# Kernel tuning notes

Measured on AMD Instinct MI355X. Metric: run time of the kernel, lower is better.

The kernel has to match this reference:

```python
import jax, jax.numpy as jnp
import numpy as np

EPS = 1e-5

def group_norm(x, gamma, beta):
    # GroupNorm(1, C) on [N, C]: normalize over channel dim per sample
    mu = jnp.mean(x, axis=-1, keepdims=True)
    var = jnp.var(x, axis=-1, keepdims=True)
    return (x - mu) * jax.lax.rsqrt(var + EPS) * gamma + beta

def setup_inputs() -> dict:
    key = jax.random.key(0)
    ks = jax.random.split(key, 4)
    T, B, I, H = 2048, 64, 256, 512
    s1 = 1.0 / np.sqrt(H + I)
    s2 = 1.0 / np.sqrt(H)
    return {
        "input": jax.random.normal(ks[0], (T, B, I), dtype=jnp.float32),
        "W1": jax.random.uniform(ks[1], (H, H + I), jnp.float32, -s1, s1),
        "g1": jnp.ones((H,), jnp.float32), "b1": jnp.zeros((H,), jnp.float32),
        "W2": jax.random.uniform(ks[2], (H, H), jnp.float32, -s2, s2),
        "g2": jnp.ones((H,), jnp.float32), "b2": jnp.zeros((H,), jnp.float32),
        "W3": jax.random.uniform(ks[3], (3 * H, H), jnp.float32, -s2, s2),
        "g3": jnp.ones((3 * H,), jnp.float32), "b3": jnp.zeros((3 * H,), jnp.float32),
    }

def reference(input, W1, g1, b1, W2, g2, b2, W3, g3, b3):
    T, B, I = input.shape
    H = W1.shape[0]

    def step(c, x):
        z = jnp.concatenate([x, c], axis=1)              # [B, I+H]
        h = jax.nn.elu(group_norm(z @ W1.T, g1, b1))     # [B, H]
        h = jax.nn.elu(group_norm(h @ W2.T, g2, b2))     # [B, H]
        o = group_norm(h @ W3.T, g3, b3)                 # [B, 3H]
        new_hx, new_cx, forget = o[:, :H], o[:, H:2*H], o[:, 2*H:]
        f = jax.nn.sigmoid(forget) ** 2                  # sigmoid_pow(x, 2)
        retain = 1.0 - f
        hx = jax.nn.elu(new_hx)
        cx = jax.nn.elu(new_cx)
        c_new = f * cx + retain * c
        return c_new, hx

    c0 = jnp.zeros((B, H), dtype=input.dtype)
    c_final, outputs = jax.lax.scan(step, c0, input)
    return outputs, c_final[None]
```

## Files before the change

### kernel.cpp

```cpp
#include <hip/hip_runtime.h>
#include <math.h>

#define T_STEPS 2048
#define BATCH   64
#define IDIM    256
#define HDIM    512
#define K1      768
#define H3      1536
#define NGROUP  4
#define NSLICE  32
#define RPG     16
#define THREADS 512

#define OFF_A1  0
#define OFF_A2  32768
#define OFF_CB  65536
#define OFF_P3  98304
#define OFF_ST  102400

typedef __attribute__((ext_vector_type(8))) __bf16 bf16x8;
typedef __attribute__((ext_vector_type(4))) float f32x4;

__device__ __forceinline__ f32x4 MFMA(bf16x8 a, bf16x8 b, f32x4 c) {
    return __builtin_amdgcn_mfma_f32_16x16x32_bf16(a, b, c, 0, 0, 0);
}

__device__ __forceinline__ float gload(const float* p) {
    return __hip_atomic_load(p, __ATOMIC_RELAXED, __HIP_MEMORY_SCOPE_AGENT);
}
__device__ __forceinline__ void gstore(float* p, float v) {
    __hip_atomic_store(p, v, __ATOMIC_RELAXED, __HIP_MEMORY_SCOPE_AGENT);
}
__device__ __forceinline__ float2 gload2(const float* p) {
    unsigned long long v = __hip_atomic_load((const unsigned long long*)p,
                                             __ATOMIC_RELAXED, __HIP_MEMORY_SCOPE_AGENT);
    return __builtin_bit_cast(float2, v);
}
__device__ __forceinline__ void gstore2(float* p, float a, float b) {
    float2 v = {a, b};
    __hip_atomic_store((unsigned long long*)p, __builtin_bit_cast(unsigned long long, v),
                       __ATOMIC_RELAXED, __HIP_MEMORY_SCOPE_AGENT);
}
__device__ __forceinline__ int gload_i(const int* p) {
    return __hip_atomic_load(p, __ATOMIC_RELAXED, __HIP_MEMORY_SCOPE_AGENT);
}
__device__ __forceinline__ unsigned gload_u(const unsigned* p) {
    return __hip_atomic_load(p, __ATOMIC_RELAXED, __HIP_MEMORY_SCOPE_AGENT);
}
__device__ __forceinline__ void gstore_us(unsigned short* p, unsigned short v) {
    __hip_atomic_store(p, v, __ATOMIC_RELAXED, __HIP_MEMORY_SCOPE_AGENT);
}

struct bf16pair { __bf16 hi, lo; };
__device__ __forceinline__ bf16pair split2(float f) {
    bf16pair r;
    r.hi = (__bf16)f;
    r.lo = (__bf16)(f - (float)r.hi);
    return r;
}
__device__ __forceinline__ unsigned pk2(float a, float b) {
    return (unsigned)__builtin_bit_cast(unsigned short, (__bf16)a) |
           ((unsigned)__builtin_bit_cast(unsigned short, (__bf16)b) << 16);
}
__device__ __forceinline__ void st_pair(__bf16* p, __bf16 a, __bf16 b) {
    unsigned v = (unsigned)__builtin_bit_cast(unsigned short, a) |
                 ((unsigned)__builtin_bit_cast(unsigned short, b) << 16);
    *(unsigned*)p = v;
}
__device__ __forceinline__ float elu1(float v) {
    return v > 0.f ? v : (expf(v) - 1.f);
}

__device__ __forceinline__ void publish(int* stamp_s, int val) {
    __syncthreads();
    if (threadIdx.x == 0)
        __hip_atomic_store(stamp_s, val, __ATOMIC_RELAXED, __HIP_MEMORY_SCOPE_AGENT);
}
__device__ __forceinline__ void poll_wave(const int* st, int target) {
    const int* p = st + (threadIdx.x & 31);
    while (true) {
        int v = gload_i(p);
        if (__all(v >= target)) break;
        __builtin_amdgcn_s_sleep(1);
    }
}

__global__ void dlstm_init(float* __restrict__ ws) {
    int idx = threadIdx.x;
    if (idx < 512) ((int*)(ws + OFF_ST))[idx] = 0;
}

__global__ __launch_bounds__(THREADS, 2) void dlstm_main(
    const float* __restrict__ x,
    const float* __restrict__ W1, const float* __restrict__ g1, const float* __restrict__ b1,
    const float* __restrict__ W2, const float* __restrict__ g2, const float* __restrict__ b2,
    const float* __restrict__ W3, const float* __restrict__ g3, const float* __restrict__ b3,
    float* __restrict__ out, float* __restrict__ ws)
{
    const int tid = threadIdx.x;
    const int bid = blockIdx.x;
    const int g = bid & 3;
    const int s = bid >> 2;
    const int r0 = g * RPG;

    const int lane = tid & 63;
    const int wv   = tid >> 6;
    const int col  = lane & 15;
    const int kq   = lane >> 4;
    const int er   = tid >> 5;
    const int l32  = tid & 31;

    float* a1 = ws + OFF_A1;
    float* a2 = ws + OFF_A2;
    unsigned short* cbu = (unsigned short*)(ws + OFF_CB);
    float* p3 = ws + OFF_P3;
    int* stb   = (int*)(ws + OFF_ST);
    int* st_a1 = stb + 0   + g * 32;
    int* st_a2 = stb + 128 + g * 32;
    int* st_p3 = stb + 256 + g * 32;
    int* st_cb = stb + 384 + g * 32;

    __shared__ __bf16 zh[16][776];
    __shared__ float comb[8][3][256];
    __shared__ float slab[16][48];
    __shared__ float stats[16][2];

    float2 g1v[8], b1v[8], g2v[8], b2v[8];
    #pragma unroll
    for (int j = 0; j < 8; ++j) {
        int k = j * 64 + l32 * 2;
        g1v[j] = *(const float2*)(g1 + k); b1v[j] = *(const float2*)(b1 + k);
        g2v[j] = *(const float2*)(g2 + k); b2v[j] = *(const float2*)(b2 + k);
    }
    float g3h = 0.f, g3c = 0.f, g3f = 0.f, b3h = 0.f, b3c = 0.f, b3f = 0.f;
    if (tid < 256) {
        int i = tid & 15; int h = 16 * s + i;
        g3h = g3[h];        g3c = g3[HDIM + h];        g3f = g3[2 * HDIM + h];
        b3h = b3[h];        b3c = b3[HDIM + h];        b3f = b3[2 * HDIM + h];
    }

    bf16x8 w1h[3], w1l[3], w2h[2], w2l[2], w3h[3][2], w3l[3][2];
    #pragma unroll
    for (int ks = 0; ks < 3; ++ks) {
        int k0 = wv * 96 + ks * 32 + kq * 8;
        const float* p = W1 + (size_t)(16 * s + col) * K1 + k0;
        #pragma unroll
        for (int e = 0; e < 8; ++e) {
            bf16pair pr = split2(p[e]);
            w1h[ks][e] = pr.hi; w1l[ks][e] = pr.lo;
        }
    }
    #pragma unroll
    for (int ks = 0; ks < 2; ++ks) {
        int k0 = wv * 64 + ks * 32 + kq * 8;
        const float* p = W2 + (size_t)(16 * s + col) * HDIM + k0;
        #pragma unroll
        for (int e = 0; e < 8; ++e) {
            bf16pair pr = split2(p[e]);
            w2h[ks][e] = pr.hi; w2l[ks][e] = pr.lo;
        }
    }
    #pragma unroll
    for (int tb = 0; tb < 3; ++tb) {
        #pragma unroll
        for (int ks = 0; ks < 2; ++ks) {
            int k0 = wv * 64 + ks * 32 + kq * 8;
            const float* p = W3 + (size_t)(tb * HDIM + 16 * s + col) * HDIM + k0;
            #pragma unroll
            for (int e = 0; e < 8; ++e) {
                bf16pair pr = split2(p[e]);
                w3h[tb][ks][e] = pr.hi; w3l[tb][ks][e] = pr.lo;
            }
        }
    }

    float creg = 0.f;

    float2 xr[4];
    unsigned xb[4];
    {
        const float* xrow = x + (size_t)(r0 + er) * IDIM;
        #pragma unroll
        for (int j = 0; j < 4; ++j) xr[j] = *(const float2*)(xrow + j * 64 + l32 * 2);
        #pragma unroll
        for (int j = 0; j < 4; ++j) xb[j] = pk2(xr[j].x, xr[j].y);
    }

    #pragma unroll 1
    for (int t = 0; t < T_STEPS; ++t) {
        unsigned* zrow = (unsigned*)&zh[er][0];
        #pragma unroll
        for (int j = 0; j < 4; ++j) zrow[j * 32 + l32] = xb[j];
        __syncthreads();
        f32x4 acc = {0.f, 0.f, 0.f, 0.f};
        #pragma unroll
        for (int ks = 0; ks < 3; ++ks) {
            int kb = wv * 96 + ks * 32;
            if (kb < IDIM) {
                bf16x8 ah = *(const bf16x8*)&zh[col][kb + kq * 8];
                acc = MFMA(ah, w1h[ks], acc);
                acc = MFMA(ah, w1l[ks], acc);
            }
        }
        if (t > 0) {
            poll_wave(st_cb, t);
            const unsigned* cbrow = (const unsigned*)cbu + (size_t)(r0 + er) * (HDIM / 2);
            #pragma unroll
            for (int j = 0; j < 8; ++j)
                zrow[128 + j * 32 + l32] = gload_u(cbrow + j * 32 + l32);
        } else {
            #pragma unroll
            for (int j = 0; j < 8; ++j) zrow[128 + j * 32 + l32] = 0u;
        }
        __syncthreads();
        #pragma unroll
        for (int ks = 0; ks < 3; ++ks) {
            int kb = wv * 96 + ks * 32;
            if (kb >= IDIM) {
                bf16x8 ah = *(const bf16x8*)&zh[col][kb + kq * 8];
                acc = MFMA(ah, w1h[ks], acc);
                acc = MFMA(ah, w1l[ks], acc);
            }
        }
        #pragma unroll
        for (int i = 0; i < 4; ++i) comb[wv][0][(kq * 4 + i) * 16 + col] = acc[i];
        __syncthreads();
        if (tid < 128) {
            int r = tid >> 3, fp = tid & 7;
            int i0 = r * 16 + fp * 2;
            float v0 = 0.f, v1 = 0.f;
            #pragma unroll
            for (int w = 0; w < 8; ++w) { v0 += comb[w][0][i0]; v1 += comb[w][0][i0 + 1]; }
            gstore2(&a1[(size_t)(r0 + r) * HDIM + 16 * s + fp * 2], v0, v1);
        }
        publish(&st_a1[s], t + 1);

        poll_wave(st_a1, t + 1);
        {
            size_t arow = (size_t)(r0 + er) * HDIM;
            float2 va[8]; float s1 = 0.f, s2 = 0.f;
            #pragma unroll
            for (int j = 0; j < 8; ++j) {
                va[j] = gload2(a1 + arow + j * 64 + l32 * 2);
                s1 += va[j].x + va[j].y; s2 += va[j].x * va[j].x + va[j].y * va[j].y;
            }
            s1 += __shfl_xor(s1, 1, 64); s2 += __shfl_xor(s2, 1, 64);
            s1 += __shfl_xor(s1, 2, 64); s2 += __shfl_xor(s2, 2, 64);
            s1 += __shfl_xor(s1, 4, 64); s2 += __shfl_xor(s2, 4, 64);
            s1 += __shfl_xor(s1, 8, 64); s2 += __shfl_xor(s2, 8, 64);
            s1 += __shfl_xor(s1, 16, 64); s2 += __shfl_xor(s2, 16, 64);
            float mu = s1 * (1.f / HDIM);
            float var = s2 * (1.f / HDIM) - mu * mu;
            float rs = rsqrtf(var + 1e-5f);
            #pragma unroll
            for (int j = 0; j < 8; ++j) {
                int k = j * 64 + l32 * 2;
                float v0 = elu1((va[j].x - mu) * rs * g1v[j].x + b1v[j].x);
                float v1 = elu1((va[j].y - mu) * rs * g1v[j].y + b1v[j].y);
                st_pair(&zh[er][k], (__bf16)v0, (__bf16)v1);
            }
        }
        __syncthreads();
        {
            f32x4 acc2 = {0.f, 0.f, 0.f, 0.f};
            #pragma unroll
            for (int ks = 0; ks < 2; ++ks) {
                int k0 = wv * 64 + ks * 32 + kq * 8;
                bf16x8 ah = *(const bf16x8*)&zh[col][k0];
                acc2 = MFMA(ah, w2h[ks], acc2);
                acc2 = MFMA(ah, w2l[ks], acc2);
            }
            #pragma unroll
            for (int i = 0; i < 4; ++i) comb[wv][0][(kq * 4 + i) * 16 + col] = acc2[i];
        }
        __syncthreads();
        if (tid < 128) {
            int r = tid >> 3, fp = tid & 7;
            int i0 = r * 16 + fp * 2;
            float v0 = 0.f, v1 = 0.f;
            #pragma unroll
            for (int w = 0; w < 8; ++w) { v0 += comb[w][0][i0]; v1 += comb[w][0][i0 + 1]; }
            gstore2(&a2[(size_t)(r0 + r) * HDIM + 16 * s + fp * 2], v0, v1);
        }
        publish(&st_a2[s], t + 1);

        poll_wave(st_a2, t + 1);
        {
            size_t arow = (size_t)(r0 + er) * HDIM;
            float2 va[8]; float s1 = 0.f, s2 = 0.f;
            #pragma unroll
            for (int j = 0; j < 8; ++j) va[j] = gload2(a2 + arow + j * 64 + l32 * 2);
            {
                int tn = (t + 1 < T_STEPS) ? t + 1 : t;
                const float* xrow = x + ((size_t)tn * BATCH + r0 + er) * IDIM;
                #pragma unroll
                for (int j = 0; j < 4; ++j) xr[j] = *(const float2*)(xrow + j * 64 + l32 * 2);
            }
            #pragma unroll
            for (int j = 0; j < 8; ++j) {
                s1 += va[j].x + va[j].y; s2 += va[j].x * va[j].x + va[j].y * va[j].y;
            }
            s1 += __shfl_xor(s1, 1, 64); s2 += __shfl_xor(s2, 1, 64);
            s1 += __shfl_xor(s1, 2, 64); s2 += __shfl_xor(s2, 2, 64);
            s1 += __shfl_xor(s1, 4, 64); s2 += __shfl_xor(s2, 4, 64);
            s1 += __shfl_xor(s1, 8, 64); s2 += __shfl_xor(s2, 8, 64);
            s1 += __shfl_xor(s1, 16, 64); s2 += __shfl_xor(s2, 16, 64);
            float mu = s1 * (1.f / HDIM);
            float var = s2 * (1.f / HDIM) - mu * mu;
            float rs = rsqrtf(var + 1e-5f);
            #pragma unroll
            for (int j = 0; j < 8; ++j) {
                int k = j * 64 + l32 * 2;
                float v0 = elu1((va[j].x - mu) * rs * g2v[j].x + b2v[j].x);
                float v1 = elu1((va[j].y - mu) * rs * g2v[j].y + b2v[j].y);
                st_pair(&zh[er][k], (__bf16)v0, (__bf16)v1);
            }
        }
        __syncthreads();
        {
            f32x4 acc0 = {0.f,0.f,0.f,0.f}, acc1 = {0.f,0.f,0.f,0.f}, acc2 = {0.f,0.f,0.f,0.f};
            #pragma unroll
            for (int ks = 0; ks < 2; ++ks) {
                int k0 = wv * 64 + ks * 32 + kq * 8;
                bf16x8 ah = *(const bf16x8*)&zh[col][k0];
                acc0 = MFMA(ah, w3h[0][ks], acc0);
                acc0 = MFMA(ah, w3l[0][ks], acc0);
                acc1 = MFMA(ah, w3h[1][ks], acc1);
                acc1 = MFMA(ah, w3l[1][ks], acc1);
                acc2 = MFMA(ah, w3h[2][ks], acc2);
                acc2 = MFMA(ah, w3l[2][ks], acc2);
            }
            #pragma unroll
            for (int i = 0; i < 4; ++i) {
                comb[wv][0][(kq * 4 + i) * 16 + col] = acc0[i];
                comb[wv][1][(kq * 4 + i) * 16 + col] = acc1[i];
                comb[wv][2][(kq * 4 + i) * 16 + col] = acc2[i];
            }
        }
        __syncthreads();
        if (tid < 384) {
            int o = tid * 2;
            int tb = o >> 8, idx = o & 255;
            int r = idx >> 4, f0 = idx & 15;
            float v0 = 0.f, v1 = 0.f;
            #pragma unroll
            for (int w = 0; w < 8; ++w) { v0 += comb[w][tb][idx]; v1 += comb[w][tb][idx + 1]; }
            slab[r][tb * 16 + f0] = v0;
            slab[r][tb * 16 + f0 + 1] = v1;
        }
        __syncthreads();
        {
            float va_ = slab[er][l32];
            float vb_ = (l32 < 16) ? slab[er][32 + l32] : 0.f;
            float s1 = va_ + vb_;
            float s2 = va_ * va_ + vb_ * vb_;
            s1 += __shfl_xor(s1, 1, 64); s2 += __shfl_xor(s2, 1, 64);
            s1 += __shfl_xor(s1, 2, 64); s2 += __shfl_xor(s2, 2, 64);
            s1 += __shfl_xor(s1, 4, 64); s2 += __shfl_xor(s2, 4, 64);
            s1 += __shfl_xor(s1, 8, 64); s2 += __shfl_xor(s2, 8, 64);
            s1 += __shfl_xor(s1, 16, 64); s2 += __shfl_xor(s2, 16, 64);
            if (l32 == 0) gstore2(&p3[((size_t)(r0 + er) * NSLICE + s) * 2], s1, s2);
        }
        publish(&st_p3[s], t + 1);

        poll_wave(st_p3, t + 1);
        {
            float2 pv = gload2(&p3[((size_t)(r0 + er) * NSLICE + l32) * 2]);
            float s1 = pv.x, s2 = pv.y;
            s1 += __shfl_xor(s1, 1, 64); s2 += __shfl_xor(s2, 1, 64);
            s1 += __shfl_xor(s1, 2, 64); s2 += __shfl_xor(s2, 2, 64);
            s1 += __shfl_xor(s1, 4, 64); s2 += __shfl_xor(s2, 4, 64);
            s1 += __shfl_xor(s1, 8, 64); s2 += __shfl_xor(s2, 8, 64);
            s1 += __shfl_xor(s1, 16, 64); s2 += __shfl_xor(s2, 16, 64);
            float mu = s1 * (1.f / H3);
            float var = s2 * (1.f / H3) - mu * mu;
            float rs = rsqrtf(var + 1e-5f);
            if (l32 == 0) { stats[er][0] = mu; stats[er][1] = rs; }
        }
        __syncthreads();
        if (tid < 256) {
            int r = tid >> 4, i = tid & 15;
            int h = 16 * s + i;
            float mu = stats[r][0], rs = stats[r][1];
            float ohn = (slab[r][i]      - mu) * rs * g3h + b3h;
            float ocn = (slab[r][16 + i] - mu) * rs * g3c + b3c;
            float ofn = (slab[r][32 + i] - mu) * rs * g3f + b3f;
            float sig = 1.f / (1.f + expf(-ofn));
            float fv = sig * sig;
            float cnew = fv * elu1(ocn) + (1.f - fv) * creg;
            creg = cnew;
            out[((size_t)t * BATCH + r0 + r) * HDIM + h] = elu1(ohn);
            gstore_us(&cbu[(size_t)(r0 + r) * HDIM + h],
                      __builtin_bit_cast(unsigned short, (__bf16)cnew));
            if (t == T_STEPS - 1)
                out[(size_t)T_STEPS * BATCH * HDIM + (size_t)(r0 + r) * HDIM + h] = cnew;
        }
        #pragma unroll
        for (int j = 0; j < 4; ++j) xb[j] = pk2(xr[j].x, xr[j].y);
        publish(&st_cb[s], t + 1);
    }
}

extern "C" void kernel_launch(void* const* d_in, const int* in_sizes, int n_in,
                              void* d_out, int out_size, void* d_ws, size_t ws_size,
                              hipStream_t stream) {
    const float* x  = (const float*)d_in[0];
    const float* W1 = (const float*)d_in[1];
    const float* g1 = (const float*)d_in[2];
    const float* b1 = (const float*)d_in[3];
    const float* W2 = (const float*)d_in[4];
    const float* g2 = (const float*)d_in[5];
    const float* b2 = (const float*)d_in[6];
    const float* W3 = (const float*)d_in[7];
    const float* g3 = (const float*)d_in[8];
    const float* b3 = (const float*)d_in[9];
    float* out = (float*)d_out;
    float* ws  = (float*)d_ws;

    dlstm_init<<<1, 512, 0, stream>>>(ws);
    dlstm_main<<<NGROUP * NSLICE, THREADS, 0, stream>>>(x, W1, g1, b1, W2, g2, b2, W3, g3, b3, out, ws);
}
```

Before: 25.98 ms.

## Replace stamp-based flag barriers with NaN-poisoned triple-buffered data polling

Drops the separate per-slice stamp counters and their publish/poll round trips. Consumers now poll the data buffers themselves, which are triple-buffered across timesteps and reset to a NaN poison value one phase ahead. Each step therefore skips a __syncthreads plus flag store and a dependent flag read before the data read. The epilogue also packs two channels per thread so c is written as one 32-bit bf16 pair. The scheme assumes real activations are never NaN or equal to the poison bit pattern. It also adds extra poison stores and a larger workspace that must be initialised.

```diff
diff --git a/kernel.cpp b/kernel.cpp
--- a/kernel.cpp
+++ b/kernel.cpp
@@ -12,11 +12,16 @@
 #define RPG     16
 #define THREADS 512
 
+#define POISON_U 0x7FC07FC0u
+
+#define A1_PH   32768
 #define OFF_A1  0
-#define OFF_A2  32768
-#define OFF_CB  65536
-#define OFF_P3  98304
-#define OFF_ST  102400
+#define OFF_A2  98304
+#define CB_PH   16384
+#define OFF_CB  196608
+#define P3_PH   4096
+#define OFF_P3  245760
+#define WS_DWORDS 258048
 
 typedef __attribute__((ext_vector_type(8))) __bf16 bf16x8;
 typedef __attribute__((ext_vector_type(4))) float f32x4;
@@ -25,12 +30,6 @@
     return __builtin_amdgcn_mfma_f32_16x16x32_bf16(a, b, c, 0, 0, 0);
 }
 
-__device__ __forceinline__ float gload(const float* p) {
-    return __hip_atomic_load(p, __ATOMIC_RELAXED, __HIP_MEMORY_SCOPE_AGENT);
-}
-__device__ __forceinline__ void gstore(float* p, float v) {
-    __hip_atomic_store(p, v, __ATOMIC_RELAXED, __HIP_MEMORY_SCOPE_AGENT);
-}
 __device__ __forceinline__ float2 gload2(const float* p) {
     unsigned long long v = __hip_atomic_load((const unsigned long long*)p,
                                              __ATOMIC_RELAXED, __HIP_MEMORY_SCOPE_AGENT);
@@ -41,13 +40,10 @@
     __hip_atomic_store((unsigned long long*)p, __builtin_bit_cast(unsigned long long, v),
                        __ATOMIC_RELAXED, __HIP_MEMORY_SCOPE_AGENT);
 }
-__device__ __forceinline__ int gload_i(const int* p) {
-    return __hip_atomic_load(p, __ATOMIC_RELAXED, __HIP_MEMORY_SCOPE_AGENT);
-}
 __device__ __forceinline__ unsigned gload_u(const unsigned* p) {
     return __hip_atomic_load(p, __ATOMIC_RELAXED, __HIP_MEMORY_SCOPE_AGENT);
 }
-__device__ __forceinline__ void gstore_us(unsigned short* p, unsigned short v) {
+__device__ __forceinline__ void gstore_u(unsigned* p, unsigned v) {
     __hip_atomic_store(p, v, __ATOMIC_RELAXED, __HIP_MEMORY_SCOPE_AGENT);
 }
 
@@ -71,23 +67,11 @@
     return v > 0.f ? v : (expf(v) - 1.f);
 }
 
-__device__ __forceinline__ void publish(int* stamp_s, int val) {
-    __syncthreads();
-    if (threadIdx.x == 0)
-        __hip_atomic_store(stamp_s, val, __ATOMIC_RELAXED, __HIP_MEMORY_SCOPE_AGENT);
-}
-__device__ __forceinline__ void poll_wave(const int* st, int target) {
-    const int* p = st + (threadIdx.x & 31);
-    while (true) {
-        int v = gload_i(p);
-        if (__all(v >= target)) break;
-        __builtin_amdgcn_s_sleep(1);
-    }
-}
-
 __global__ void dlstm_init(float* __restrict__ ws) {
-    int idx = threadIdx.x;
-    if (idx < 512) ((int*)(ws + OFF_ST))[idx] = 0;
+    unsigned* w = (unsigned*)ws;
+    for (unsigned i = blockIdx.x * blockDim.x + threadIdx.x; i < WS_DWORDS;
+         i += gridDim.x * blockDim.x)
+        w[i] = POISON_U;
 }
 
 __global__ __launch_bounds__(THREADS, 2) void dlstm_main(
@@ -110,20 +94,17 @@
     const int er   = tid >> 5;
     const int l32  = tid & 31;
 
-    float* a1 = ws + OFF_A1;
-    float* a2 = ws + OFF_A2;
-    unsigned short* cbu = (unsigned short*)(ws + OFF_CB);
-    float* p3 = ws + OFF_P3;
-    int* stb   = (int*)(ws + OFF_ST);
-    int* st_a1 = stb + 0   + g * 32;
-    int* st_a2 = stb + 128 + g * 32;
-    int* st_p3 = stb + 256 + g * 32;
-    int* st_cb = stb + 384 + g * 32;
+    float*    a1base = ws + OFF_A1;
+    float*    a2base = ws + OFF_A2;
+    unsigned* cbbase = (unsigned*)ws + OFF_CB;
+    float*    p3base = ws + OFF_P3;
 
     __shared__ __bf16 zh[16][776];
     __shared__ float comb[8][3][256];
     __shared__ float slab[16][48];
     __shared__ float stats[16][2];
+
+    const float qnan = __builtin_bit_cast(float, POISON_U);
 
     float2 g1v[8], b1v[8], g2v[8], b2v[8];
     #pragma unroll
@@ -132,11 +113,12 @@
         g1v[j] = *(const float2*)(g1 + k); b1v[j] = *(const float2*)(b1 + k);
         g2v[j] = *(const float2*)(g2 + k); b2v[j] = *(const float2*)(b2 + k);
     }
-    float g3h = 0.f, g3c = 0.f, g3f = 0.f, b3h = 0.f, b3c = 0.f, b3f = 0.f;
-    if (tid < 256) {
-        int i = tid & 15; int h = 16 * s + i;
-        g3h = g3[h];        g3c = g3[HDIM + h];        g3f = g3[2 * HDIM + h];
-        b3h = b3[h];        b3c = b3[HDIM + h];        b3f = b3[2 * HDIM + h];
+    float2 g3h2 = {0,0}, b3h2 = {0,0}, g3c2 = {0,0}, b3c2 = {0,0}, g3f2 = {0,0}, b3f2 = {0,0};
+    if (tid < 128) {
+        int j = tid & 7; int h0 = 16 * s + 2 * j;
+        g3h2 = *(const float2*)(g3 + h0);            b3h2 = *(const float2*)(b3 + h0);
+        g3c2 = *(const float2*)(g3 + HDIM + h0);     b3c2 = *(const float2*)(b3 + HDIM + h0);
+        g3f2 = *(const float2*)(g3 + 2 * HDIM + h0); b3f2 = *(const float2*)(b3 + 2 * HDIM + h0);
     }
 
     bf16x8 w1h[3], w1l[3], w2h[2], w2l[2], w3h[3][2], w3l[3][2];
@@ -174,7 +156,7 @@
         }
     }
 
-    float creg = 0.f;
+    float cr0 = 0.f, cr1 = 0.f;
 
     float2 xr[4];
     unsigned xb[4];
@@ -188,6 +170,20 @@
 
     #pragma unroll 1
     for (int t = 0; t < T_STEPS; ++t) {
+        const int ph  = t % 3;
+        const int ph1 = (ph == 2) ? 0 : ph + 1;
+        const int ph2 = (ph == 0) ? 2 : ph - 1;
+
+        float*    a1w = a1base + ph  * A1_PH;
+        float*    a1p = a1base + ph2 * A1_PH;
+        float*    a2w = a2base + ph  * A1_PH;
+        float*    a2p = a2base + ph2 * A1_PH;
+        unsigned* cbw = cbbase + ph  * CB_PH;
+        unsigned* cbp = cbbase + ph1 * CB_PH;
+        const unsigned* cbr = cbbase + ph2 * CB_PH;
+        float*    p3w = p3base + ph  * P3_PH;
+        float*    p3p = p3base + ph2 * P3_PH;
+
         unsigned* zrow = (unsigned*)&zh[er][0];
         #pragma unroll
         for (int j = 0; j < 4; ++j) zrow[j * 32 + l32] = xb[j];
@@ -203,11 +199,20 @@
             }
         }
         if (t > 0) {
-            poll_wave(st_cb, t);
-            const unsigned* cbrow = (const unsigned*)cbu + (size_t)(r0 + er) * (HDIM / 2);
-            #pragma unroll
-            for (int j = 0; j < 8; ++j)
-                zrow[128 + j * 32 + l32] = gload_u(cbrow + j * 32 + l32);
+            const unsigned* cbrow = cbr + (size_t)(r0 + er) * (HDIM / 2);
+            unsigned vb[8]; unsigned m = 0xffu;
+            while (true) {
+                #pragma unroll
+                for (int j = 0; j < 8; ++j)
+                    if (m & (1u << j)) {
+                        vb[j] = gload_u(cbrow + j * 32 + l32);
+                        if (vb[j] != POISON_U) m &= ~(1u << j);
+                    }
+                if (__all(m == 0)) break;
+                __builtin_amdgcn_s_sleep(1);
+            }
+            #pragma unroll
+            for (int j = 0; j < 8; ++j) zrow[128 + j * 32 + l32] = vb[j];
         } else {
             #pragma unroll
             for (int j = 0; j < 8; ++j) zrow[128 + j * 32 + l32] = 0u;
@@ -231,17 +236,27 @@
             float v0 = 0.f, v1 = 0.f;
             #pragma unroll
             for (int w = 0; w < 8; ++w) { v0 += comb[w][0][i0]; v1 += comb[w][0][i0 + 1]; }
-            gstore2(&a1[(size_t)(r0 + r) * HDIM + 16 * s + fp * 2], v0, v1);
-        }
-        publish(&st_a1[s], t + 1);
-
-        poll_wave(st_a1, t + 1);
-        {
-            size_t arow = (size_t)(r0 + er) * HDIM;
-            float2 va[8]; float s1 = 0.f, s2 = 0.f;
+            size_t o = (size_t)(r0 + r) * HDIM + 16 * s + fp * 2;
+            gstore2(a1w + o, v0, v1);
+            gstore2(a1p + o, qnan, qnan);
+        }
+
+        {
+            const float* arow = a1w + (size_t)(r0 + er) * HDIM;
+            float2 va[8]; unsigned m = 0xffu;
+            while (true) {
+                #pragma unroll
+                for (int j = 0; j < 8; ++j)
+                    if (m & (1u << j)) {
+                        va[j] = gload2(arow + j * 64 + l32 * 2);
+                        if (va[j].x == va[j].x) m &= ~(1u << j);
+                    }
+                if (__all(m == 0)) break;
+                __builtin_amdgcn_s_sleep(1);
+            }
+            float s1 = 0.f, s2 = 0.f;
             #pragma unroll
             for (int j = 0; j < 8; ++j) {
-                va[j] = gload2(a1 + arow + j * 64 + l32 * 2);
                 s1 += va[j].x + va[j].y; s2 += va[j].x * va[j].x + va[j].y * va[j].y;
             }
             s1 += __shfl_xor(s1, 1, 64); s2 += __shfl_xor(s2, 1, 64);
@@ -280,22 +295,31 @@
             float v0 = 0.f, v1 = 0.f;
             #pragma unroll
             for (int w = 0; w < 8; ++w) { v0 += comb[w][0][i0]; v1 += comb[w][0][i0 + 1]; }
-            gstore2(&a2[(size_t)(r0 + r) * HDIM + 16 * s + fp * 2], v0, v1);
-        }
-        publish(&st_a2[s], t + 1);
-
-        poll_wave(st_a2, t + 1);
-        {
-            size_t arow = (size_t)(r0 + er) * HDIM;
-            float2 va[8]; float s1 = 0.f, s2 = 0.f;
-            #pragma unroll
-            for (int j = 0; j < 8; ++j) va[j] = gload2(a2 + arow + j * 64 + l32 * 2);
+            size_t o = (size_t)(r0 + r) * HDIM + 16 * s + fp * 2;
+            gstore2(a2w + o, v0, v1);
+            gstore2(a2p + o, qnan, qnan);
+        }
+
+        {
             {
                 int tn = (t + 1 < T_STEPS) ? t + 1 : t;
                 const float* xrow = x + ((size_t)tn * BATCH + r0 + er) * IDIM;
                 #pragma unroll
                 for (int j = 0; j < 4; ++j) xr[j] = *(const float2*)(xrow + j * 64 + l32 * 2);
             }
+            const float* arow = a2w + (size_t)(r0 + er) * HDIM;
+            float2 va[8]; unsigned m = 0xffu;
+            while (true) {
+                #pragma unroll
+                for (int j = 0; j < 8; ++j)
+                    if (m & (1u << j)) {
+                        va[j] = gload2(arow + j * 64 + l32 * 2);
+                        if (va[j].x == va[j].x) m &= ~(1u << j);
+                    }
+                if (__all(m == 0)) break;
+                __builtin_amdgcn_s_sleep(1);
+            }
+            float s1 = 0.f, s2 = 0.f;
             #pragma unroll
             for (int j = 0; j < 8; ++j) {
                 s1 += va[j].x + va[j].y; s2 += va[j].x * va[j].x + va[j].y * va[j].y;
@@ -359,13 +383,21 @@
             s1 += __shfl_xor(s1, 4, 64); s2 += __shfl_xor(s2, 4, 64);
             s1 += __shfl_xor(s1, 8, 64); s2 += __shfl_xor(s2, 8, 64);
             s1 += __shfl_xor(s1, 16, 64); s2 += __shfl_xor(s2, 16, 64);
-            if (l32 == 0) gstore2(&p3[((size_t)(r0 + er) * NSLICE + s) * 2], s1, s2);
-        }
-        publish(&st_p3[s], t + 1);
-
-        poll_wave(st_p3, t + 1);
-        {
-            float2 pv = gload2(&p3[((size_t)(r0 + er) * NSLICE + l32) * 2]);
+            if (l32 == 0) {
+                size_t o = ((size_t)(r0 + er) * NSLICE + s) * 2;
+                gstore2(p3w + o, s1, s2);
+                gstore2(p3p + o, qnan, qnan);
+            }
+        }
+
+        {
+            const float* pp = p3w + ((size_t)(r0 + er) * NSLICE + l32) * 2;
+            float2 pv;
+            while (true) {
+                pv = gload2(pp);
+                if (__all(pv.x == pv.x)) break;
+                __builtin_amdgcn_s_sleep(1);
+            }
             float s1 = pv.x, s2 = pv.y;
             s1 += __shfl_xor(s1, 1, 64); s2 += __shfl_xor(s2, 1, 64);
             s1 += __shfl_xor(s1, 2, 64); s2 += __shfl_xor(s2, 2, 64);
@@ -378,26 +410,34 @@
             if (l32 == 0) { stats[er][0] = mu; stats[er][1] = rs; }
         }
         __syncthreads();
-        if (tid < 256) {
-            int r = tid >> 4, i = tid & 15;
-            int h = 16 * s + i;
+        if (tid < 128) {
+            int r = tid >> 3, j = tid & 7;
+            int i0 = 2 * j;
             float mu = stats[r][0], rs = stats[r][1];
-            float ohn = (slab[r][i]      - mu) * rs * g3h + b3h;
-            float ocn = (slab[r][16 + i] - mu) * rs * g3c + b3c;
-            float ofn = (slab[r][32 + i] - mu) * rs * g3f + b3f;
-            float sig = 1.f / (1.f + expf(-ofn));
-            float fv = sig * sig;
-            float cnew = fv * elu1(ocn) + (1.f - fv) * creg;
-            creg = cnew;
-            out[((size_t)t * BATCH + r0 + r) * HDIM + h] = elu1(ohn);
-            gstore_us(&cbu[(size_t)(r0 + r) * HDIM + h],
-                      __builtin_bit_cast(unsigned short, (__bf16)cnew));
-            if (t == T_STEPS - 1)
-                out[(size_t)T_STEPS * BATCH * HDIM + (size_t)(r0 + r) * HDIM + h] = cnew;
+            float oh0 = (slab[r][i0]          - mu) * rs * g3h2.x + b3h2.x;
+            float oh1 = (slab[r][i0 + 1]      - mu) * rs * g3h2.y + b3h2.y;
+            float oc0 = (slab[r][16 + i0]     - mu) * rs * g3c2.x + b3c2.x;
+            float oc1 = (slab[r][16 + i0 + 1] - mu) * rs * g3c2.y + b3c2.y;
+            float of0 = (slab[r][32 + i0]     - mu) * rs * g3f2.x + b3f2.x;
+            float of1 = (slab[r][32 + i0 + 1] - mu) * rs * g3f2.y + b3f2.y;
+            float sg0 = 1.f / (1.f + expf(-of0)); float f0 = sg0 * sg0;
+            float sg1 = 1.f / (1.f + expf(-of1)); float f1 = sg1 * sg1;
+            float cn0 = f0 * elu1(oc0) + (1.f - f0) * cr0;
+            float cn1 = f1 * elu1(oc1) + (1.f - f1) * cr1;
+            cr0 = cn0; cr1 = cn1;
+            size_t co = (size_t)(r0 + r) * (HDIM / 2) + 8 * s + j;
+            gstore_u(cbw + co, pk2(cn0, cn1));
+            gstore_u(cbp + co, POISON_U);
+            float2 ho = { elu1(oh0), elu1(oh1) };
+            *(float2*)(out + ((size_t)t * BATCH + r0 + r) * HDIM + 16 * s + i0) = ho;
+            if (t == T_STEPS - 1) {
+                float2 cf = { cn0, cn1 };
+                *(float2*)(out + (size_t)T_STEPS * BATCH * HDIM
+                               + (size_t)(r0 + r) * HDIM + 16 * s + i0) = cf;
+            }
         }
         #pragma unroll
         for (int j = 0; j < 4; ++j) xb[j] = pk2(xr[j].x, xr[j].y);
-        publish(&st_cb[s], t + 1);
     }
 }
 
@@ -417,6 +457,6 @@
     float* out = (float*)d_out;
     float* ws  = (float*)d_ws;
 
-    dlstm_init<<<1, 512, 0, stream>>>(ws);
+    dlstm_init<<<256, 256, 0, stream>>>(ws);
     dlstm_main<<<NGROUP * NSLICE, THREADS, 0, stream>>>(x, W1, g1, b1, W2, g2, b2, W3, g3, b3, out, ws);
 }
```

Measured after the change: 32.94 ms. +26.8%, slower.

## Drop the cell-state exchange barrier by recomputing the full cell state per block

Applied to the files above, without the earlier changes.

Each block now writes its pre-norm cell and forget slices to workspace. After the third-layer stats barrier, every block reads the whole 512-wide rows and updates the complete cell state for its 16 rows in registers, writing it straight into shared memory. This removes the per-step bf16 cell-state broadcast and its grid-wide barrier, leaving three cross-block syncs per step instead of four. The per-block stamp arrays with 32-lane polling are replaced by shared atomic counters that each wave increments and that are polled by a single load. The cost is redundant elementwise work, extra global traffic for the oc/of buffers, and atomic contention on the counters.

```diff
diff --git a/kernel.cpp b/kernel.cpp
--- a/kernel.cpp
+++ b/kernel.cpp
@@ -12,11 +12,14 @@
 #define RPG     16
 #define THREADS 512
 
-#define OFF_A1  0
-#define OFF_A2  32768
-#define OFF_CB  65536
-#define OFF_P3  98304
-#define OFF_ST  102400
+
+#define OFF_A1 0
+#define OFF_A2 32768
+#define OFF_OC 65536
+#define OFF_OF 98304
+#define OFF_P3 131072
+#define OFF_CT 135168
+#define N_CT   768
 
 typedef __attribute__((ext_vector_type(8))) __bf16 bf16x8;
 typedef __attribute__((ext_vector_type(4))) float f32x4;
@@ -25,12 +28,6 @@
     return __builtin_amdgcn_mfma_f32_16x16x32_bf16(a, b, c, 0, 0, 0);
 }
 
-__device__ __forceinline__ float gload(const float* p) {
-    return __hip_atomic_load(p, __ATOMIC_RELAXED, __HIP_MEMORY_SCOPE_AGENT);
-}
-__device__ __forceinline__ void gstore(float* p, float v) {
-    __hip_atomic_store(p, v, __ATOMIC_RELAXED, __HIP_MEMORY_SCOPE_AGENT);
-}
 __device__ __forceinline__ float2 gload2(const float* p) {
     unsigned long long v = __hip_atomic_load((const unsigned long long*)p,
                                              __ATOMIC_RELAXED, __HIP_MEMORY_SCOPE_AGENT);
@@ -43,12 +40,6 @@
 }
 __device__ __forceinline__ int gload_i(const int* p) {
     return __hip_atomic_load(p, __ATOMIC_RELAXED, __HIP_MEMORY_SCOPE_AGENT);
-}
-__device__ __forceinline__ unsigned gload_u(const unsigned* p) {
-    return __hip_atomic_load(p, __ATOMIC_RELAXED, __HIP_MEMORY_SCOPE_AGENT);
-}
-__device__ __forceinline__ void gstore_us(unsigned short* p, unsigned short v) {
-    __hip_atomic_store(p, v, __ATOMIC_RELAXED, __HIP_MEMORY_SCOPE_AGENT);
 }
 
 struct bf16pair { __bf16 hi, lo; };
@@ -71,23 +62,18 @@
     return v > 0.f ? v : (expf(v) - 1.f);
 }
 
-__device__ __forceinline__ void publish(int* stamp_s, int val) {
-    __syncthreads();
-    if (threadIdx.x == 0)
-        __hip_atomic_store(stamp_s, val, __ATOMIC_RELAXED, __HIP_MEMORY_SCOPE_AGENT);
-}
-__device__ __forceinline__ void poll_wave(const int* st, int target) {
-    const int* p = st + (threadIdx.x & 31);
-    while (true) {
-        int v = gload_i(p);
-        if (__all(v >= target)) break;
-        __builtin_amdgcn_s_sleep(1);
-    }
+__device__ __forceinline__ void wave_pub(int* c) {
+    asm volatile("s_waitcnt vmcnt(0)" ::: "memory");
+    if ((threadIdx.x & 63) == 0)
+        (void)__hip_atomic_fetch_add(c, 1, __ATOMIC_RELAXED, __HIP_MEMORY_SCOPE_AGENT);
+}
+__device__ __forceinline__ void poll_ctr(const int* c, int tgt) {
+    while (gload_i(c) < tgt) __builtin_amdgcn_s_sleep(1);
 }
 
 __global__ void dlstm_init(float* __restrict__ ws) {
     int idx = threadIdx.x;
-    if (idx < 512) ((int*)(ws + OFF_ST))[idx] = 0;
+    if (idx < N_CT) ((int*)ws + OFF_CT)[idx] = 0;
 }
 
 __global__ __launch_bounds__(THREADS, 2) void dlstm_main(
@@ -110,20 +96,26 @@
     const int er   = tid >> 5;
     const int l32  = tid & 31;
 
-    float* a1 = ws + OFF_A1;
-    float* a2 = ws + OFF_A2;
-    unsigned short* cbu = (unsigned short*)(ws + OFF_CB);
-    float* p3 = ws + OFF_P3;
-    int* stb   = (int*)(ws + OFF_ST);
-    int* st_a1 = stb + 0   + g * 32;
-    int* st_a2 = stb + 128 + g * 32;
-    int* st_p3 = stb + 256 + g * 32;
-    int* st_cb = stb + 384 + g * 32;
+    float* a1    = ws + OFF_A1;
+    float* a2    = ws + OFF_A2;
+    float* oc_ws = ws + OFF_OC;
+    float* of_ws = ws + OFF_OF;
+    float* p3    = ws + OFF_P3;
+    int*   ctb   = (int*)ws + OFF_CT + g * 192;
+    int*   ctA   = ctb;
+    int*   ctB   = ctb + 64;
+    int*   ctC   = ctb + 128;
 
     __shared__ __bf16 zh[16][776];
     __shared__ float comb[8][3][256];
     __shared__ float slab[16][48];
     __shared__ float stats[16][2];
+    __shared__ float g3c_s[512], b3c_s[512], g3f_s[512], b3f_s[512];
+
+    {
+        g3c_s[tid] = g3[HDIM + tid];     b3c_s[tid] = b3[HDIM + tid];
+        g3f_s[tid] = g3[2 * HDIM + tid]; b3f_s[tid] = b3[2 * HDIM + tid];
+    }
 
     float2 g1v[8], b1v[8], g2v[8], b2v[8];
     #pragma unroll
@@ -132,11 +124,10 @@
         g1v[j] = *(const float2*)(g1 + k); b1v[j] = *(const float2*)(b1 + k);
         g2v[j] = *(const float2*)(g2 + k); b2v[j] = *(const float2*)(b2 + k);
     }
-    float g3h = 0.f, g3c = 0.f, g3f = 0.f, b3h = 0.f, b3c = 0.f, b3f = 0.f;
+    float g3h = 0.f, b3h = 0.f;
     if (tid < 256) {
-        int i = tid & 15; int h = 16 * s + i;
-        g3h = g3[h];        g3c = g3[HDIM + h];        g3f = g3[2 * HDIM + h];
-        b3h = b3[h];        b3c = b3[HDIM + h];        b3f = b3[2 * HDIM + h];
+        int i = tid & 15;
+        g3h = g3[16 * s + i]; b3h = b3[16 * s + i];
     }
 
     bf16x8 w1h[3], w1l[3], w2h[2], w2l[2], w3h[3][2], w3l[3][2];
@@ -174,7 +165,12 @@
         }
     }
 
-    float creg = 0.f;
+    float cr[8][2];
+    #pragma unroll
+    for (int k = 0; k < 8; ++k) { cr[k][0] = 0.f; cr[k][1] = 0.f; }
+    #pragma unroll
+    for (int k = 0; k < 8; ++k)
+        st_pair(&zh[er][256 + 2 * l32 + 64 * k], (__bf16)0.f, (__bf16)0.f);
 
     float2 xr[4];
     unsigned xb[4];
@@ -192,38 +188,17 @@
         #pragma unroll
         for (int j = 0; j < 4; ++j) zrow[j * 32 + l32] = xb[j];
         __syncthreads();
-        f32x4 acc = {0.f, 0.f, 0.f, 0.f};
-        #pragma unroll
-        for (int ks = 0; ks < 3; ++ks) {
-            int kb = wv * 96 + ks * 32;
-            if (kb < IDIM) {
-                bf16x8 ah = *(const bf16x8*)&zh[col][kb + kq * 8];
+        {
+            f32x4 acc = {0.f, 0.f, 0.f, 0.f};
+            #pragma unroll
+            for (int ks = 0; ks < 3; ++ks) {
+                bf16x8 ah = *(const bf16x8*)&zh[col][wv * 96 + ks * 32 + kq * 8];
                 acc = MFMA(ah, w1h[ks], acc);
                 acc = MFMA(ah, w1l[ks], acc);
             }
-        }
-        if (t > 0) {
-            poll_wave(st_cb, t);
-            const unsigned* cbrow = (const unsigned*)cbu + (size_t)(r0 + er) * (HDIM / 2);
-            #pragma unroll
-            for (int j = 0; j < 8; ++j)
-                zrow[128 + j * 32 + l32] = gload_u(cbrow + j * 32 + l32);
-        } else {
-            #pragma unroll
-            for (int j = 0; j < 8; ++j) zrow[128 + j * 32 + l32] = 0u;
-        }
-        __syncthreads();
-        #pragma unroll
-        for (int ks = 0; ks < 3; ++ks) {
-            int kb = wv * 96 + ks * 32;
-            if (kb >= IDIM) {
-                bf16x8 ah = *(const bf16x8*)&zh[col][kb + kq * 8];
-                acc = MFMA(ah, w1h[ks], acc);
-                acc = MFMA(ah, w1l[ks], acc);
-            }
-        }
-        #pragma unroll
-        for (int i = 0; i < 4; ++i) comb[wv][0][(kq * 4 + i) * 16 + col] = acc[i];
+            #pragma unroll
+            for (int i = 0; i < 4; ++i) comb[wv][0][(kq * 4 + i) * 16 + col] = acc[i];
+        }
         __syncthreads();
         if (tid < 128) {
             int r = tid >> 3, fp = tid & 7;
@@ -232,10 +207,10 @@
             #pragma unroll
             for (int w = 0; w < 8; ++w) { v0 += comb[w][0][i0]; v1 += comb[w][0][i0 + 1]; }
             gstore2(&a1[(size_t)(r0 + r) * HDIM + 16 * s + fp * 2], v0, v1);
-        }
-        publish(&st_a1[s], t + 1);
-
-        poll_wave(st_a1, t + 1);
+            wave_pub(ctA);
+        }
+
+        poll_ctr(ctA, 64 * (t + 1));
         {
             size_t arow = (size_t)(r0 + er) * HDIM;
             float2 va[8]; float s1 = 0.f, s2 = 0.f;
@@ -281,21 +256,21 @@
             #pragma unroll
             for (int w = 0; w < 8; ++w) { v0 += comb[w][0][i0]; v1 += comb[w][0][i0 + 1]; }
             gstore2(&a2[(size_t)(r0 + r) * HDIM + 16 * s + fp * 2], v0, v1);
-        }
-        publish(&st_a2[s], t + 1);
-
-        poll_wave(st_a2, t + 1);
-        {
-            size_t arow = (size_t)(r0 + er) * HDIM;
-            float2 va[8]; float s1 = 0.f, s2 = 0.f;
-            #pragma unroll
-            for (int j = 0; j < 8; ++j) va[j] = gload2(a2 + arow + j * 64 + l32 * 2);
+            wave_pub(ctB);
+        }
+
+        poll_ctr(ctB, 64 * (t + 1));
+        {
             {
                 int tn = (t + 1 < T_STEPS) ? t + 1 : t;
                 const float* xrow = x + ((size_t)tn * BATCH + r0 + er) * IDIM;
                 #pragma unroll
                 for (int j = 0; j < 4; ++j) xr[j] = *(const float2*)(xrow + j * 64 + l32 * 2);
             }
+            size_t arow = (size_t)(r0 + er) * HDIM;
+            float2 va[8]; float s1 = 0.f, s2 = 0.f;
+            #pragma unroll
+            for (int j = 0; j < 8; ++j) va[j] = gload2(a2 + arow + j * 64 + l32 * 2);
             #pragma unroll
             for (int j = 0; j < 8; ++j) {
                 s1 += va[j].x + va[j].y; s2 += va[j].x * va[j].x + va[j].y * va[j].y;
@@ -345,8 +320,12 @@
             float v0 = 0.f, v1 = 0.f;
             #pragma unroll
             for (int w = 0; w < 8; ++w) { v0 += comb[w][tb][idx]; v1 += comb[w][tb][idx + 1]; }
-            slab[r][tb * 16 + f0] = v0;
+            slab[r][tb * 16 + f0]     = v0;
             slab[r][tb * 16 + f0 + 1] = v1;
+            if (tb == 1)
+                gstore2(&oc_ws[(size_t)(r0 + r) * HDIM + 16 * s + f0], v0, v1);
+            else if (tb == 2)
+                gstore2(&of_ws[(size_t)(r0 + r) * HDIM + 16 * s + f0], v0, v1);
         }
         __syncthreads();
         {
@@ -361,9 +340,19 @@
             s1 += __shfl_xor(s1, 16, 64); s2 += __shfl_xor(s2, 16, 64);
             if (l32 == 0) gstore2(&p3[((size_t)(r0 + er) * NSLICE + s) * 2], s1, s2);
         }
-        publish(&st_p3[s], t + 1);
-
-        poll_wave(st_p3, t + 1);
+        wave_pub(ctC);
+
+        poll_ctr(ctC, 256 * (t + 1));
+        float2 ocv[8], ofv[8];
+        {
+            const float* ocr = oc_ws + (size_t)(r0 + er) * HDIM + 2 * l32;
+            const float* ofr = of_ws + (size_t)(r0 + er) * HDIM + 2 * l32;
+            #pragma unroll
+            for (int k = 0; k < 8; ++k) {
+                ocv[k] = gload2(ocr + 64 * k);
+                ofv[k] = gload2(ofr + 64 * k);
+            }
+        }
         {
             float2 pv = gload2(&p3[((size_t)(r0 + er) * NSLICE + l32) * 2]);
             float s1 = pv.x, s2 = pv.y;
@@ -378,26 +367,40 @@
             if (l32 == 0) { stats[er][0] = mu; stats[er][1] = rs; }
         }
         __syncthreads();
+        {
+            float mu = stats[er][0], rs = stats[er][1];
+            #pragma unroll
+            for (int k = 0; k < 8; ++k) {
+                int c0k = 2 * l32 + 64 * k;
+                float2 gc = *(const float2*)&g3c_s[c0k];
+                float2 bc = *(const float2*)&b3c_s[c0k];
+                float2 gf = *(const float2*)&g3f_s[c0k];
+                float2 bf = *(const float2*)&b3f_s[c0k];
+                float ocn0 = (ocv[k].x - mu) * rs * gc.x + bc.x;
+                float ocn1 = (ocv[k].y - mu) * rs * gc.y + bc.y;
+                float ofn0 = (ofv[k].x - mu) * rs * gf.x + bf.x;
+                float ofn1 = (ofv[k].y - mu) * rs * gf.y + bf.y;
+                float sg0 = 1.f / (1.f + expf(-ofn0)); float f0 = sg0 * sg0;
+                float sg1 = 1.f / (1.f + expf(-ofn1)); float f1 = sg1 * sg1;
+                float cn0 = f0 * elu1(ocn0) + (1.f - f0) * cr[k][0];
+                float cn1 = f1 * elu1(ocn1) + (1.f - f1) * cr[k][1];
+                cr[k][0] = cn0; cr[k][1] = cn1;
+                st_pair(&zh[er][256 + c0k], (__bf16)cn0, (__bf16)cn1);
+                if (t == T_STEPS - 1) {
+                    float2 cf = {cn0, cn1};
+                    *(float2*)(out + (size_t)T_STEPS * BATCH * HDIM
+                                   + (size_t)(r0 + er) * HDIM + c0k) = cf;
+                }
+            }
+        }
         if (tid < 256) {
             int r = tid >> 4, i = tid & 15;
-            int h = 16 * s + i;
             float mu = stats[r][0], rs = stats[r][1];
-            float ohn = (slab[r][i]      - mu) * rs * g3h + b3h;
-            float ocn = (slab[r][16 + i] - mu) * rs * g3c + b3c;
-            float ofn = (slab[r][32 + i] - mu) * rs * g3f + b3f;
-            float sig = 1.f / (1.f + expf(-ofn));
-            float fv = sig * sig;
-            float cnew = fv * elu1(ocn) + (1.f - fv) * creg;
-            creg = cnew;
-            out[((size_t)t * BATCH + r0 + r) * HDIM + h] = elu1(ohn);
-            gstore_us(&cbu[(size_t)(r0 + r) * HDIM + h],
-                      __builtin_bit_cast(unsigned short, (__bf16)cnew));
-            if (t == T_STEPS - 1)
-                out[(size_t)T_STEPS * BATCH * HDIM + (size_t)(r0 + r) * HDIM + h] = cnew;
+            float oh = (slab[r][i] - mu) * rs * g3h + b3h;
+            out[((size_t)t * BATCH + r0 + r) * HDIM + 16 * s + i] = elu1(oh);
         }
         #pragma unroll
         for (int j = 0; j < 4; ++j) xb[j] = pk2(xr[j].x, xr[j].y);
-        publish(&st_cb[s], t + 1);
     }
 }
 
@@ -417,6 +420,6 @@
     float* out = (float*)d_out;
     float* ws  = (float*)d_ws;
 
-    dlstm_init<<<1, 512, 0, stream>>>(ws);
+    dlstm_init<<<1, 768, 0, stream>>>(ws);
     dlstm_main<<<NGROUP * NSLICE, THREADS, 0, stream>>>(x, W1, g1, b1, W2, g2, b2, W3, g3, b3, out, ws);
 }
```

After: 52.72 ms. +102.9%, slower.

## Replace block barriers before stamp publish with per-wave LDS counters and overlap x-MFMA

Applied to the files above, without the earlier changes.

Each inter-block stamp publish now uses a per-wave LDS atomic counter: the last wave to arrive writes the global stamp, replacing a full __syncthreads before the store. The input-projection MFMA for the next step is moved into the wait for the p3 stats so it overlaps the cross-block latency. The cell-state bf16 publish now happens before the output store, which shortens the critical path. The workspace offsets shrink. The scheme relies on s_waitcnt vmcnt(0) ordering without release semantics, which carries a memory-ordering risk.

```diff
diff --git a/kernel.cpp b/kernel.cpp
--- a/kernel.cpp
+++ b/kernel.cpp
@@ -12,11 +12,13 @@
 #define RPG     16
 #define THREADS 512
 
+
 #define OFF_A1  0
 #define OFF_A2  32768
 #define OFF_CB  65536
-#define OFF_P3  98304
-#define OFF_ST  102400
+#define OFF_P3  81920
+#define OFF_ST  86016
+#define N_ST    512
 
 typedef __attribute__((ext_vector_type(8))) __bf16 bf16x8;
 typedef __attribute__((ext_vector_type(4))) float f32x4;
@@ -25,12 +27,6 @@
     return __builtin_amdgcn_mfma_f32_16x16x32_bf16(a, b, c, 0, 0, 0);
 }
 
-__device__ __forceinline__ float gload(const float* p) {
-    return __hip_atomic_load(p, __ATOMIC_RELAXED, __HIP_MEMORY_SCOPE_AGENT);
-}
-__device__ __forceinline__ void gstore(float* p, float v) {
-    __hip_atomic_store(p, v, __ATOMIC_RELAXED, __HIP_MEMORY_SCOPE_AGENT);
-}
 __device__ __forceinline__ float2 gload2(const float* p) {
     unsigned long long v = __hip_atomic_load((const unsigned long long*)p,
                                              __ATOMIC_RELAXED, __HIP_MEMORY_SCOPE_AGENT);
@@ -48,6 +44,9 @@
     return __hip_atomic_load(p, __ATOMIC_RELAXED, __HIP_MEMORY_SCOPE_AGENT);
 }
 __device__ __forceinline__ void gstore_us(unsigned short* p, unsigned short v) {
+    __hip_atomic_store(p, v, __ATOMIC_RELAXED, __HIP_MEMORY_SCOPE_AGENT);
+}
+__device__ __forceinline__ void gstore_stamp(int* p, int v) {
     __hip_atomic_store(p, v, __ATOMIC_RELAXED, __HIP_MEMORY_SCOPE_AGENT);
 }
 
@@ -71,10 +70,13 @@
     return v > 0.f ? v : (expf(v) - 1.f);
 }
 
-__device__ __forceinline__ void publish(int* stamp_s, int val) {
-    __syncthreads();
-    if (threadIdx.x == 0)
-        __hip_atomic_store(stamp_s, val, __ATOMIC_RELAXED, __HIP_MEMORY_SCOPE_AGENT);
+__device__ __forceinline__ void wave_pub(int* lds_ctr, int finish_old, int* stamp, int val) {
+    asm volatile("s_waitcnt vmcnt(0)" ::: "memory");
+    if ((threadIdx.x & 63) == 0) {
+        int old = __hip_atomic_fetch_add(lds_ctr, 1, __ATOMIC_RELAXED,
+                                         __HIP_MEMORY_SCOPE_WORKGROUP);
+        if (old == finish_old) gstore_stamp(stamp, val);
+    }
 }
 __device__ __forceinline__ void poll_wave(const int* st, int target) {
     const int* p = st + (threadIdx.x & 31);
@@ -87,7 +89,7 @@
 
 __global__ void dlstm_init(float* __restrict__ ws) {
     int idx = threadIdx.x;
-    if (idx < 512) ((int*)(ws + OFF_ST))[idx] = 0;
+    if (idx < N_ST) ((int*)ws + OFF_ST)[idx] = 0;
 }
 
 __global__ __launch_bounds__(THREADS, 2) void dlstm_main(
@@ -114,7 +116,7 @@
     float* a2 = ws + OFF_A2;
     unsigned short* cbu = (unsigned short*)(ws + OFF_CB);
     float* p3 = ws + OFF_P3;
-    int* stb   = (int*)(ws + OFF_ST);
+    int* stb   = (int*)ws + OFF_ST;
     int* st_a1 = stb + 0   + g * 32;
     int* st_a2 = stb + 128 + g * 32;
     int* st_p3 = stb + 256 + g * 32;
@@ -124,6 +126,9 @@
     __shared__ float comb[8][3][256];
     __shared__ float slab[16][48];
     __shared__ float stats[16][2];
+    __shared__ int syncc[4];
+
+    if (tid < 4) syncc[tid] = 0;
 
     float2 g1v[8], b1v[8], g2v[8], b2v[8];
     #pragma unroll
@@ -176,41 +181,39 @@
 
     float creg = 0.f;
 
+    #pragma unroll
+    for (int k = 0; k < 8; ++k)
+        st_pair(&zh[er][256 + 2 * l32 + 64 * k], (__bf16)0.f, (__bf16)0.f);
     float2 xr[4];
-    unsigned xb[4];
     {
         const float* xrow = x + (size_t)(r0 + er) * IDIM;
         #pragma unroll
         for (int j = 0; j < 4; ++j) xr[j] = *(const float2*)(xrow + j * 64 + l32 * 2);
-        #pragma unroll
-        for (int j = 0; j < 4; ++j) xb[j] = pk2(xr[j].x, xr[j].y);
+        unsigned* zrow = (unsigned*)&zh[er][0];
+        #pragma unroll
+        for (int j = 0; j < 4; ++j) zrow[j * 32 + l32] = pk2(xr[j].x, xr[j].y);
+    }
+    __syncthreads();
+    f32x4 acc = {0.f, 0.f, 0.f, 0.f};
+    #pragma unroll
+    for (int ks = 0; ks < 3; ++ks) {
+        int kb = wv * 96 + ks * 32;
+        if (kb < IDIM) {
+            bf16x8 ah = *(const bf16x8*)&zh[col][kb + kq * 8];
+            acc = MFMA(ah, w1h[ks], acc);
+            acc = MFMA(ah, w1l[ks], acc);
+        }
     }
 
     #pragma unroll 1
     for (int t = 0; t < T_STEPS; ++t) {
         unsigned* zrow = (unsigned*)&zh[er][0];
-        #pragma unroll
-        for (int j = 0; j < 4; ++j) zrow[j * 32 + l32] = xb[j];
-        __syncthreads();
-        f32x4 acc = {0.f, 0.f, 0.f, 0.f};
-        #pragma unroll
-        for (int ks = 0; ks < 3; ++ks) {
-            int kb = wv * 96 + ks * 32;
-            if (kb < IDIM) {
-                bf16x8 ah = *(const bf16x8*)&zh[col][kb + kq * 8];
-                acc = MFMA(ah, w1h[ks], acc);
-                acc = MFMA(ah, w1l[ks], acc);
-            }
-        }
         if (t > 0) {
             poll_wave(st_cb, t);
             const unsigned* cbrow = (const unsigned*)cbu + (size_t)(r0 + er) * (HDIM / 2);
             #pragma unroll
             for (int j = 0; j < 8; ++j)
                 zrow[128 + j * 32 + l32] = gload_u(cbrow + j * 32 + l32);
-        } else {
-            #pragma unroll
-            for (int j = 0; j < 8; ++j) zrow[128 + j * 32 + l32] = 0u;
         }
         __syncthreads();
         #pragma unroll
@@ -232,8 +235,8 @@
             #pragma unroll
             for (int w = 0; w < 8; ++w) { v0 += comb[w][0][i0]; v1 += comb[w][0][i0 + 1]; }
             gstore2(&a1[(size_t)(r0 + r) * HDIM + 16 * s + fp * 2], v0, v1);
-        }
-        publish(&st_a1[s], t + 1);
+            wave_pub(&syncc[0], 2 * t + 1, &st_a1[s], t + 1);
+        }
 
         poll_wave(st_a1, t + 1);
         {
@@ -281,21 +284,21 @@
             #pragma unroll
             for (int w = 0; w < 8; ++w) { v0 += comb[w][0][i0]; v1 += comb[w][0][i0 + 1]; }
             gstore2(&a2[(size_t)(r0 + r) * HDIM + 16 * s + fp * 2], v0, v1);
-        }
-        publish(&st_a2[s], t + 1);
+            wave_pub(&syncc[1], 2 * t + 1, &st_a2[s], t + 1);
+        }
 
         poll_wave(st_a2, t + 1);
         {
-            size_t arow = (size_t)(r0 + er) * HDIM;
-            float2 va[8]; float s1 = 0.f, s2 = 0.f;
-            #pragma unroll
-            for (int j = 0; j < 8; ++j) va[j] = gload2(a2 + arow + j * 64 + l32 * 2);
             {
                 int tn = (t + 1 < T_STEPS) ? t + 1 : t;
                 const float* xrow = x + ((size_t)tn * BATCH + r0 + er) * IDIM;
                 #pragma unroll
                 for (int j = 0; j < 4; ++j) xr[j] = *(const float2*)(xrow + j * 64 + l32 * 2);
             }
+            size_t arow = (size_t)(r0 + er) * HDIM;
+            float2 va[8]; float s1 = 0.f, s2 = 0.f;
+            #pragma unroll
+            for (int j = 0; j < 8; ++j) va[j] = gload2(a2 + arow + j * 64 + l32 * 2);
             #pragma unroll
             for (int j = 0; j < 8; ++j) {
                 s1 += va[j].x + va[j].y; s2 += va[j].x * va[j].x + va[j].y * va[j].y;
@@ -347,6 +350,10 @@
             for (int w = 0; w < 8; ++w) { v0 += comb[w][tb][idx]; v1 += comb[w][tb][idx + 1]; }
             slab[r][tb * 16 + f0] = v0;
             slab[r][tb * 16 + f0 + 1] = v1;
+        }
+        {
+            #pragma unroll
+            for (int j = 0; j < 4; ++j) zrow[j * 32 + l32] = pk2(xr[j].x, xr[j].y);
         }
         __syncthreads();
         {
@@ -361,7 +368,18 @@
             s1 += __shfl_xor(s1, 16, 64); s2 += __shfl_xor(s2, 16, 64);
             if (l32 == 0) gstore2(&p3[((size_t)(r0 + er) * NSLICE + s) * 2], s1, s2);
         }
-        publish(&st_p3[s], t + 1);
+        wave_pub(&syncc[2], 8 * t + 7, &st_p3[s], t + 1);
+
+        acc[0] = 0.f; acc[1] = 0.f; acc[2] = 0.f; acc[3] = 0.f;
+        #pragma unroll
+        for (int ks = 0; ks < 3; ++ks) {
+            int kb = wv * 96 + ks * 32;
+            if (kb < IDIM) {
+                bf16x8 ah = *(const bf16x8*)&zh[col][kb + kq * 8];
+                acc = MFMA(ah, w1h[ks], acc);
+                acc = MFMA(ah, w1l[ks], acc);
+            }
+        }
 
         poll_wave(st_p3, t + 1);
         {
@@ -382,22 +400,20 @@
             int r = tid >> 4, i = tid & 15;
             int h = 16 * s + i;
             float mu = stats[r][0], rs = stats[r][1];
-            float ohn = (slab[r][i]      - mu) * rs * g3h + b3h;
             float ocn = (slab[r][16 + i] - mu) * rs * g3c + b3c;
             float ofn = (slab[r][32 + i] - mu) * rs * g3f + b3f;
             float sig = 1.f / (1.f + expf(-ofn));
             float fv = sig * sig;
             float cnew = fv * elu1(ocn) + (1.f - fv) * creg;
             creg = cnew;
-            out[((size_t)t * BATCH + r0 + r) * HDIM + h] = elu1(ohn);
             gstore_us(&cbu[(size_t)(r0 + r) * HDIM + h],
                       __builtin_bit_cast(unsigned short, (__bf16)cnew));
+            wave_pub(&syncc[3], 4 * t + 3, &st_cb[s], t + 1);
+            float ohn = (slab[r][i] - mu) * rs * g3h + b3h;
+            out[((size_t)t * BATCH + r0 + r) * HDIM + h] = elu1(ohn);
             if (t == T_STEPS - 1)
                 out[(size_t)T_STEPS * BATCH * HDIM + (size_t)(r0 + r) * HDIM + h] = cnew;
         }
-        #pragma unroll
-        for (int j = 0; j < 4; ++j) xb[j] = pk2(xr[j].x, xr[j].y);
-        publish(&st_cb[s], t + 1);
     }
 }
 
```

New measurement: 38.34 ms. 1.48x slower.
